# Kernel tuning notes

Hardware: AMD Instinct MI355X
Metric: run time of the kernel (lower is better)

## Reference

```python
import jax, jax.numpy as jnp
import numpy as np

N_HEADS = 4


def setup_inputs() -> dict:
    key = jax.random.key(0)
    ks = jax.random.split(key, 8)
    T, B, V, F = 30, 64, 32, 128   # len_pred, batch, n_vehicles, feature_size
    L, LF, TH = 64, 64, 20         # n_lanes, lane_feature_size, len_hist
    vehicles = jax.random.normal(ks[0], (T, B, V, F), dtype=jnp.float32)
    lanes = jax.random.normal(ks[1], (B, V, L, LF), dtype=jnp.float32)
    mask_lanes = jax.random.randint(ks[2], (TH, B, V, L), 0, 2).astype(bool)
    # torch Linear weight layout [out, in]; conv 1x1 weights squeezed to [out, in]
    Wk = jax.random.normal(ks[3], (F, LF), dtype=jnp.float32) / np.sqrt(LF)
    Wv = jax.random.normal(ks[4], (F, LF), dtype=jnp.float32) / np.sqrt(LF)
    Wq = jax.random.normal(ks[5], (F, F), dtype=jnp.float32) / np.sqrt(F)
    Wc = jax.random.normal(ks[6], (F, F), dtype=jnp.float32) / np.sqrt(F)
    return {"vehicles": vehicles, "lanes": lanes, "mask_lanes": mask_lanes,
            "Wk": Wk, "Wv": Wv, "Wq": Wq, "Wc": Wc}


def reference(vehicles, lanes, mask_lanes, Wk, Wv, Wq, Wc):
    # vehicles: [T,B,V,F], lanes: [B,V,L,LF], mask_lanes: [TH,B,V,L] bool
    T, B, V, F = vehicles.shape
    L = lanes.shape[2]
    H = N_HEADS
    hd = F // H
    # Linear projections of lanes (torch Linear: y = x @ W.T)
    k = jnp.einsum('bvlf,gf->bvlg', lanes, Wk).reshape(B, V, L, H, hd)
    v = jnp.einsum('bvlf,gf->bvlg', lanes, Wv).reshape(B, V, L, H, hd)
    # 1x1 Conv2d on feature channels == per-position linear
    q = jnp.einsum('tbvf,gf->tbvg', vehicles, Wq).reshape(T, B, V, H, hd)
    # mask: any over history dim -> [B,V,L] (the second any in attention is a no-op
    # since the mask is repeated identically over T and heads)
    mask = jnp.any(mask_lanes, axis=0)  # [B,V,L]
    scores = jnp.einsum('tbvhd,bvlhd->tbvhl', q, k) / jnp.sqrt(jnp.float32(hd))
    scores = jnp.where(mask[None, :, :, None, :], scores, jnp.float32(-1e9))
    p = jax.nn.softmax(scores, axis=-1)  # [T,B,V,H,L]
    out = jnp.einsum('tbvhl,bvlhd->tbvhd', p, v).reshape(T, B, V, F)
    out = jnp.einsum('tbvf,gf->tbvg', out, Wc) + vehicles
    return out
```

## Files before the change

kernel.cpp:

```cpp
#include <hip/hip_runtime.h>

#define T_  30
#define B_  64
#define V_  32
#define F_  128
#define L_  64
#define LF_ 64
#define TH_ 20
#define H_  4
#define HD_ 32

typedef __attribute__((ext_vector_type(8))) short bf16x8;
typedef __attribute__((ext_vector_type(4))) float f32x4;
#define MFMA(a,b,c) __builtin_amdgcn_mfma_f32_16x16x32_bf16(a, b, c, 0, 0, 0)

__device__ __forceinline__ float bf1(unsigned short u) {
    unsigned int x = ((unsigned int)u) << 16; float f; __builtin_memcpy(&f, &x, 4); return f;
}
__device__ __forceinline__ unsigned short f2bf(float f) {
    unsigned int x; __builtin_memcpy(&x, &f, 4);
    x += 0x7fffu + ((x >> 16) & 1u);
    return (unsigned short)(x >> 16);
}
__device__ __forceinline__ float4 ld4(const void* p, int idx4, bool isBf16) {
    if (isBf16) {
        ushort4 u = ((const ushort4*)p)[idx4];
        return make_float4(bf1(u.x), bf1(u.y), bf1(u.z), bf1(u.w));
    }
    return ((const float4*)p)[idx4];
}
__device__ __forceinline__ void st4bf(unsigned short* p, f32x4 v) {
    ushort4 u = { f2bf(v[0]), f2bf(v[1]), f2bf(v[2]), f2bf(v[3]) };
    *(ushort4*)p = u;
}
__device__ __forceinline__ bf16x8 ldWfrag(const void* W, int off, bool isBf16) {
    if (isBf16) return *(const bf16x8*)((const unsigned short*)W + off);
    const float* p = (const float*)W + off;
    float4 a = *(const float4*)p;
    float4 b = *(const float4*)(p + 4);
    bf16x8 r;
    r[0] = (short)f2bf(a.x); r[1] = (short)f2bf(a.y);
    r[2] = (short)f2bf(a.z); r[3] = (short)f2bf(a.w);
    r[4] = (short)f2bf(b.x); r[5] = (short)f2bf(b.y);
    r[6] = (short)f2bf(b.z); r[7] = (short)f2bf(b.w);
    return r;
}

__global__ __launch_bounds__(256, 2)
void lane_attn_kernel(const void* __restrict__ veh,
                      const void* __restrict__ lanes,
                      const void* __restrict__ maskp,
                      const void* __restrict__ Wk, const void* __restrict__ Wv,
                      const void* __restrict__ Wq, const void* __restrict__ Wc,
                      float* __restrict__ outp)
{
    const int bv   = blockIdx.x;
    const int tid  = threadIdx.x;
    const int w    = tid >> 6;
    const int lane = tid & 63;
    const int quad = lane >> 4;
    const int lm   = lane & 15;
    const int fbase = w * 32;

    __shared__ __align__(16) unsigned short sRegion[13824];
    __shared__ __align__(16) unsigned short sK [64 * 136];
    __shared__ __align__(16) unsigned short sVt[128 * 72];
    unsigned short* sQ     = sRegion;
    unsigned short* sO     = sRegion;
    unsigned short* sLanes = sRegion + 4352;
    unsigned short* sVehB  = sRegion + 9472;
    unsigned short* sS     = sRegion + 4352;

    const unsigned short* vh16 = (const unsigned short*)veh;
    const int field = (vh16[2 * lane] >> 7) & 0xFF;
    const bool isBf16 = __popcll(__ballot(field >= 100 && field <= 130)) >= 32;
    const unsigned char* mbp = (const unsigned char*)maskp;
    const bool maskByte = (__ballot(mbp[4 * lane + 1] != 0) != 0ULL);

    bool ok;
    {
        const int* mi = (const int*)maskp;
        int o = 0;
        #pragma unroll
        for (int th = 0; th < TH_; ++th) {
            const size_t e = (size_t)th * (B_ * V_ * L_) + (size_t)bv * L_ + lane;
            o |= maskByte ? (int)mbp[e] : mi[e];
        }
        ok = (o != 0);
    }

    bf16x8 wbK[2][2], wbV[2][2], wq[4][2];
    #pragma unroll
    for (int kt = 0; kt < 2; ++kt)
        #pragma unroll
        for (int nt = 0; nt < 2; ++nt) {
            const int off = (fbase + nt * 16 + lm) * 64 + kt * 32 + quad * 8;
            wbK[kt][nt] = ldWfrag(Wk, off, isBf16);
            wbV[kt][nt] = ldWfrag(Wv, off, isBf16);
        }
    #pragma unroll
    for (int kt = 0; kt < 4; ++kt)
        #pragma unroll
        for (int nt = 0; nt < 2; ++nt)
            wq[kt][nt] = ldWfrag(Wq, (fbase + nt * 16 + lm) * 128 + kt * 32 + quad * 8, isBf16);

    for (int u = tid; u < 64 * 16; u += 256) {
        const int l = u >> 4, c4 = u & 15;
        float4 x = ld4(lanes, bv * (L_ * LF_ / 4) + u, isBf16);
        ushort4 y = { f2bf(x.x), f2bf(x.y), f2bf(x.z), f2bf(x.w) };
        *(ushort4*)&sLanes[l * 80 + c4 * 4] = y;
    }
    for (int u = tid; u < 32 * 32; u += 256) {
        const int t = u >> 5, c4 = u & 31;
        ushort4 y = {0, 0, 0, 0};
        if (t < T_) {
            float4 x = ld4(veh, (t * (B_ * V_) + bv) * (F_ / 4) + c4, isBf16);
            y.x = f2bf(x.x); y.y = f2bf(x.y); y.z = f2bf(x.z); y.w = f2bf(x.w);
        }
        *(ushort4*)&sVehB[t * 136 + c4 * 4] = y;
    }
    __syncthreads();

    {
        f32x4 accK[2][4], accV[2][4];
        #pragma unroll
        for (int nt = 0; nt < 2; ++nt)
            #pragma unroll
            for (int mt = 0; mt < 4; ++mt) { accK[nt][mt] = (f32x4)0.f; accV[nt][mt] = (f32x4)0.f; }
        #pragma unroll
        for (int kt = 0; kt < 2; ++kt) {
            bf16x8 a[4];
            #pragma unroll
            for (int mt = 0; mt < 4; ++mt)
                a[mt] = *(const bf16x8*)&sLanes[(mt * 16 + lm) * 80 + kt * 32 + quad * 8];
            #pragma unroll
            for (int nt = 0; nt < 2; ++nt)
                #pragma unroll
                for (int mt = 0; mt < 4; ++mt) {
                    accK[nt][mt] = MFMA(a[mt], wbK[kt][nt], accK[nt][mt]);
                    accV[nt][mt] = MFMA(a[mt], wbV[kt][nt], accV[nt][mt]);
                }
        }
        #pragma unroll
        for (int nt = 0; nt < 2; ++nt) {
            const int f = fbase + nt * 16 + lm;
            #pragma unroll
            for (int mt = 0; mt < 4; ++mt) {
                const int l0 = mt * 16 + quad * 4;
                #pragma unroll
                for (int r = 0; r < 4; ++r) sK[(l0 + r) * 136 + f] = f2bf(accK[nt][mt][r]);
                st4bf(&sVt[f * 72 + l0], accV[nt][mt]);
            }
        }
    }

    {
        f32x4 acc[2][2];
        #pragma unroll
        for (int nt = 0; nt < 2; ++nt)
            #pragma unroll
            for (int mt = 0; mt < 2; ++mt) acc[nt][mt] = (f32x4)0.f;
        #pragma unroll
        for (int kt = 0; kt < 4; ++kt) {
            bf16x8 a[2];
            #pragma unroll
            for (int mt = 0; mt < 2; ++mt)
                a[mt] = *(const bf16x8*)&sVehB[(mt * 16 + lm) * 136 + kt * 32 + quad * 8];
            #pragma unroll
            for (int nt = 0; nt < 2; ++nt)
                #pragma unroll
                for (int mt = 0; mt < 2; ++mt) acc[nt][mt] = MFMA(a[mt], wq[kt][nt], acc[nt][mt]);
        }
        const float sc = 0.17677669529663687f;
        #pragma unroll
        for (int nt = 0; nt < 2; ++nt) {
            const int g = fbase + nt * 16 + lm;
            #pragma unroll
            for (int mt = 0; mt < 2; ++mt) {
                const int t0 = mt * 16 + quad * 4;
                #pragma unroll
                for (int r = 0; r < 4; ++r) sQ[(t0 + r) * 136 + g] = f2bf(acc[nt][mt][r] * sc);
            }
        }
    }

    bf16x8 wc[4][2];
    #pragma unroll
    for (int kt = 0; kt < 4; ++kt)
        #pragma unroll
        for (int nt = 0; nt < 2; ++nt)
            wc[kt][nt] = ldWfrag(Wc, (fbase + nt * 16 + lm) * 128 + kt * 32 + quad * 8, isBf16);

    __syncthreads();

    {
        bf16x8 a[4], b[2];
        #pragma unroll
        for (int mt = 0; mt < 4; ++mt)
            a[mt] = *(const bf16x8*)&sK[(mt * 16 + lm) * 136 + fbase + quad * 8];
        #pragma unroll
        for (int nt = 0; nt < 2; ++nt)
            b[nt] = *(const bf16x8*)&sQ[(nt * 16 + lm) * 136 + fbase + quad * 8];
        #pragma unroll
        for (int mt = 0; mt < 4; ++mt)
            #pragma unroll
            for (int nt = 0; nt < 2; ++nt) {
                f32x4 acc = MFMA(a[mt], b[nt], (f32x4)0.f);
                const int t = nt * 16 + lm;
                st4bf(&sS[(w * 32 + t) * 72 + mt * 16 + quad * 4], acc);
            }
    }

    {
        #pragma unroll
        for (int t = 0; t < T_; ++t) {
            const int idx = (w * 32 + t) * 72 + lane;
            const float p = ok ? __expf(bf1(sS[idx])) : 0.f;
            sS[idx] = f2bf(p);
        }
        sS[(w * 32 + 30) * 72 + lane] = 0;
        sS[(w * 32 + 31) * 72 + lane] = 0;
    }

    {
        bf16x8 bones;
        #pragma unroll
        for (int j = 0; j < 8; ++j) bones[j] = (short)0x3F80;
        f32x4 acc[2][2], ssum[2];
        #pragma unroll
        for (int mt = 0; mt < 2; ++mt) {
            ssum[mt] = (f32x4)0.f;
            #pragma unroll
            for (int nt = 0; nt < 2; ++nt) acc[mt][nt] = (f32x4)0.f;
        }
        #pragma unroll
        for (int kt = 0; kt < 2; ++kt) {
            bf16x8 a[2], b[2];
            #pragma unroll
            for (int mt = 0; mt < 2; ++mt)
                a[mt] = *(const bf16x8*)&sS[(w * 32 + mt * 16 + lm) * 72 + kt * 32 + quad * 8];
            #pragma unroll
            for (int nt = 0; nt < 2; ++nt)
                b[nt] = *(const bf16x8*)&sVt[(fbase + nt * 16 + lm) * 72 + kt * 32 + quad * 8];
            #pragma unroll
            for (int mt = 0; mt < 2; ++mt) {
                ssum[mt] = MFMA(a[mt], bones, ssum[mt]);
                #pragma unroll
                for (int nt = 0; nt < 2; ++nt) acc[mt][nt] = MFMA(a[mt], b[nt], acc[mt][nt]);
            }
        }
        #pragma unroll
        for (int mt = 0; mt < 2; ++mt)
            #pragma unroll
            for (int r = 0; r < 4; ++r) {
                const float s = ssum[mt][r];
                const float inv = (s > 0.f) ? 1.f / s : 0.f;
                const int t = mt * 16 + quad * 4 + r;
                #pragma unroll
                for (int nt = 0; nt < 2; ++nt)
                    sO[t * 136 + fbase + nt * 16 + lm] = f2bf(acc[mt][nt][r] * inv);
            }
    }

    float res[2][2][4];
    #pragma unroll
    for (int nt = 0; nt < 2; ++nt) {
        const int g = fbase + nt * 16 + lm;
        #pragma unroll
        for (int mt = 0; mt < 2; ++mt)
            #pragma unroll
            for (int r = 0; r < 4; ++r) {
                const int t = mt * 16 + quad * 4 + r;
                float v = 0.f;
                if (t < T_) {
                    const size_t off = ((size_t)t * (B_ * V_) + bv) * F_ + g;
                    v = isBf16 ? bf1(((const unsigned short*)veh)[off])
                               : ((const float*)veh)[off];
                }
                res[nt][mt][r] = v;
            }
    }
    __syncthreads();

    {
        f32x4 acc[2][2];
        #pragma unroll
        for (int nt = 0; nt < 2; ++nt)
            #pragma unroll
            for (int mt = 0; mt < 2; ++mt) acc[nt][mt] = (f32x4)0.f;
        #pragma unroll
        for (int kt = 0; kt < 4; ++kt) {
            bf16x8 a[2];
            #pragma unroll
            for (int mt = 0; mt < 2; ++mt)
                a[mt] = *(const bf16x8*)&sO[(mt * 16 + lm) * 136 + kt * 32 + quad * 8];
            #pragma unroll
            for (int nt = 0; nt < 2; ++nt)
                #pragma unroll
                for (int mt = 0; mt < 2; ++mt) acc[nt][mt] = MFMA(a[mt], wc[kt][nt], acc[nt][mt]);
        }
        #pragma unroll
        for (int nt = 0; nt < 2; ++nt) {
            const int g = fbase + nt * 16 + lm;
            #pragma unroll
            for (int mt = 0; mt < 2; ++mt)
                #pragma unroll
                for (int r = 0; r < 4; ++r) {
                    const int t = mt * 16 + quad * 4 + r;
                    if (t < T_) {
                        const size_t off = ((size_t)t * (B_ * V_) + bv) * F_ + g;
                        outp[off] = acc[nt][mt][r] + res[nt][mt][r];
                    }
                }
        }
    }
}

extern "C" void kernel_launch(void* const* d_in, const int* in_sizes, int n_in,
                              void* d_out, int out_size, void* d_ws, size_t ws_size,
                              hipStream_t stream) {
    (void)in_sizes; (void)n_in; (void)out_size; (void)d_ws; (void)ws_size;
    lane_attn_kernel<<<dim3(B_ * V_), dim3(256), 0, stream>>>(
        d_in[0], d_in[1], d_in[2], d_in[3], d_in[4], d_in[5], d_in[6],
        (float*)d_out);
}
```

Baseline: 186.3 us.

## Restructure lane attention into per-wave private smem with swizzled layouts and fewer barriers

Each wave now loads its MFMA operand fragments for lanes and vehicles straight from global memory instead of staging them through shared memory. K, Q, V and probabilities go into per-wave XOR-swizzled shared buffers, which removes the first barrier and avoids bank conflicts. The softmax exponent is applied directly on the score accumulators using a ballot mask, removing a shared-memory round trip. Shared memory shrinks and launch bounds rise to 4 blocks per CU. The risks are redundant global loads, since each wave reloads the same lanes and vehicles tiles, and register pressure from the higher occupancy target.

```diff
diff --git a/kernel.cpp b/kernel.cpp
--- a/kernel.cpp
+++ b/kernel.cpp
@@ -1,4 +1,5 @@
 #include <hip/hip_runtime.h>
+#include <hip/hip_bf16.h>
 
 #define T_  30
 #define B_  64
@@ -22,31 +23,20 @@
     x += 0x7fffu + ((x >> 16) & 1u);
     return (unsigned short)(x >> 16);
 }
-__device__ __forceinline__ float4 ld4(const void* p, int idx4, bool isBf16) {
-    if (isBf16) {
-        ushort4 u = ((const ushort4*)p)[idx4];
-        return make_float4(bf1(u.x), bf1(u.y), bf1(u.z), bf1(u.w));
-    }
-    return ((const float4*)p)[idx4];
-}
-__device__ __forceinline__ void st4bf(unsigned short* p, f32x4 v) {
-    ushort4 u = { f2bf(v[0]), f2bf(v[1]), f2bf(v[2]), f2bf(v[3]) };
-    *(ushort4*)p = u;
-}
-__device__ __forceinline__ bf16x8 ldWfrag(const void* W, int off, bool isBf16) {
-    if (isBf16) return *(const bf16x8*)((const unsigned short*)W + off);
-    const float* p = (const float*)W + off;
-    float4 a = *(const float4*)p;
-    float4 b = *(const float4*)(p + 4);
-    bf16x8 r;
-    r[0] = (short)f2bf(a.x); r[1] = (short)f2bf(a.y);
-    r[2] = (short)f2bf(a.z); r[3] = (short)f2bf(a.w);
-    r[4] = (short)f2bf(b.x); r[5] = (short)f2bf(b.y);
-    r[6] = (short)f2bf(b.z); r[7] = (short)f2bf(b.w);
-    return r;
-}
-
-__global__ __launch_bounds__(256, 2)
+__device__ __forceinline__ unsigned int pkbf(float a, float b) {
+    __hip_bfloat162 h = __float22bfloat162_rn(make_float2(a, b));
+    unsigned int u; __builtin_memcpy(&u, &h, 4); return u;
+}
+__device__ __forceinline__ bf16x8 ldfrag(const void* p, size_t elem, bool isBf16) {
+    if (isBf16) return *(const bf16x8*)((const unsigned short*)p + elem);
+    const float* f = (const float*)p + elem;
+    float4 a = *(const float4*)f;
+    float4 b = *(const float4*)(f + 4);
+    uint4 u = { pkbf(a.x, a.y), pkbf(a.z, a.w), pkbf(b.x, b.y), pkbf(b.z, b.w) };
+    bf16x8 r; __builtin_memcpy(&r, &u, 16); return r;
+}
+
+__global__ __launch_bounds__(256, 4)
 void lane_attn_kernel(const void* __restrict__ veh,
                       const void* __restrict__ lanes,
                       const void* __restrict__ maskp,
@@ -62,22 +52,17 @@
     const int lm   = lane & 15;
     const int fbase = w * 32;
 
-    __shared__ __align__(16) unsigned short sRegion[13824];
-    __shared__ __align__(16) unsigned short sK [64 * 136];
-    __shared__ __align__(16) unsigned short sVt[128 * 72];
-    unsigned short* sQ     = sRegion;
-    unsigned short* sO     = sRegion;
-    unsigned short* sLanes = sRegion + 4352;
-    unsigned short* sVehB  = sRegion + 9472;
-    unsigned short* sS     = sRegion + 4352;
+    __shared__ __align__(16) unsigned short S[20480];
+    const int kb = w * 3072, qb = kb + 2048, vb = 12288 + w * 2048;
+    const int pb = kb, ob = 12288;
 
     const unsigned short* vh16 = (const unsigned short*)veh;
-    const int field = (vh16[2 * lane] >> 7) & 0xFF;
-    const bool isBf16 = __popcll(__ballot(field >= 100 && field <= 130)) >= 32;
+    const int fld = (vh16[2 * lane] >> 7) & 0xFF;
+    const bool isBf16 = __popcll(__ballot(fld >= 100 && fld <= 130)) >= 32;
     const unsigned char* mbp = (const unsigned char*)maskp;
     const bool maskByte = (__ballot(mbp[4 * lane + 1] != 0) != 0ULL);
 
-    bool ok;
+    unsigned long long okmask;
     {
         const int* mi = (const int*)maskp;
         int o = 0;
@@ -86,75 +71,88 @@
             const size_t e = (size_t)th * (B_ * V_ * L_) + (size_t)bv * L_ + lane;
             o |= maskByte ? (int)mbp[e] : mi[e];
         }
-        ok = (o != 0);
-    }
-
-    bf16x8 wbK[2][2], wbV[2][2], wq[4][2];
-    #pragma unroll
-    for (int kt = 0; kt < 2; ++kt)
-        #pragma unroll
-        for (int nt = 0; nt < 2; ++nt) {
-            const int off = (fbase + nt * 16 + lm) * 64 + kt * 32 + quad * 8;
-            wbK[kt][nt] = ldWfrag(Wk, off, isBf16);
-            wbV[kt][nt] = ldWfrag(Wv, off, isBf16);
-        }
-    #pragma unroll
-    for (int kt = 0; kt < 4; ++kt)
-        #pragma unroll
-        for (int nt = 0; nt < 2; ++nt)
-            wq[kt][nt] = ldWfrag(Wq, (fbase + nt * 16 + lm) * 128 + kt * 32 + quad * 8, isBf16);
-
-    for (int u = tid; u < 64 * 16; u += 256) {
-        const int l = u >> 4, c4 = u & 15;
-        float4 x = ld4(lanes, bv * (L_ * LF_ / 4) + u, isBf16);
-        ushort4 y = { f2bf(x.x), f2bf(x.y), f2bf(x.z), f2bf(x.w) };
-        *(ushort4*)&sLanes[l * 80 + c4 * 4] = y;
-    }
-    for (int u = tid; u < 32 * 32; u += 256) {
-        const int t = u >> 5, c4 = u & 31;
-        ushort4 y = {0, 0, 0, 0};
-        if (t < T_) {
-            float4 x = ld4(veh, (t * (B_ * V_) + bv) * (F_ / 4) + c4, isBf16);
-            y.x = f2bf(x.x); y.y = f2bf(x.y); y.z = f2bf(x.z); y.w = f2bf(x.w);
-        }
-        *(ushort4*)&sVehB[t * 136 + c4 * 4] = y;
-    }
-    __syncthreads();
-
-    {
-        f32x4 accK[2][4], accV[2][4];
-        #pragma unroll
-        for (int nt = 0; nt < 2; ++nt)
-            #pragma unroll
-            for (int mt = 0; mt < 4; ++mt) { accK[nt][mt] = (f32x4)0.f; accV[nt][mt] = (f32x4)0.f; }
+        okmask = __ballot(o != 0);
+    }
+
+    {
+        bf16x8 wb[2][2];
+        #pragma unroll
+        for (int kt = 0; kt < 2; ++kt)
+            #pragma unroll
+            for (int nt = 0; nt < 2; ++nt)
+                wb[kt][nt] = ldfrag(Wk, (size_t)(fbase + nt * 16 + lm) * LF_ + kt * 32 + quad * 8, isBf16);
+        f32x4 acc[2][4];
+        #pragma unroll
+        for (int nt = 0; nt < 2; ++nt)
+            #pragma unroll
+            for (int mt = 0; mt < 4; ++mt) acc[nt][mt] = (f32x4)0.f;
         #pragma unroll
         for (int kt = 0; kt < 2; ++kt) {
             bf16x8 a[4];
             #pragma unroll
             for (int mt = 0; mt < 4; ++mt)
-                a[mt] = *(const bf16x8*)&sLanes[(mt * 16 + lm) * 80 + kt * 32 + quad * 8];
-            #pragma unroll
-            for (int nt = 0; nt < 2; ++nt)
-                #pragma unroll
-                for (int mt = 0; mt < 4; ++mt) {
-                    accK[nt][mt] = MFMA(a[mt], wbK[kt][nt], accK[nt][mt]);
-                    accV[nt][mt] = MFMA(a[mt], wbV[kt][nt], accV[nt][mt]);
-                }
-        }
-        #pragma unroll
-        for (int nt = 0; nt < 2; ++nt) {
-            const int f = fbase + nt * 16 + lm;
-            #pragma unroll
-            for (int mt = 0; mt < 4; ++mt) {
-                const int l0 = mt * 16 + quad * 4;
-                #pragma unroll
-                for (int r = 0; r < 4; ++r) sK[(l0 + r) * 136 + f] = f2bf(accK[nt][mt][r]);
-                st4bf(&sVt[f * 72 + l0], accV[nt][mt]);
-            }
-        }
-    }
-
-    {
+                a[mt] = ldfrag(lanes, (size_t)(bv * L_ + mt * 16 + lm) * LF_ + kt * 32 + quad * 8, isBf16);
+            #pragma unroll
+            for (int nt = 0; nt < 2; ++nt)
+                #pragma unroll
+                for (int mt = 0; mt < 4; ++mt) acc[nt][mt] = MFMA(a[mt], wb[kt][nt], acc[nt][mt]);
+        }
+        #pragma unroll
+        for (int nt = 0; nt < 2; ++nt) {
+            const int chunkc = nt * 2 + (lm >> 3);
+            #pragma unroll
+            for (int mt = 0; mt < 4; ++mt)
+                #pragma unroll
+                for (int r = 0; r < 4; ++r) {
+                    const int l = mt * 16 + quad * 4 + r;
+                    S[kb + l * 32 + ((chunkc ^ (l & 3)) << 3) + (lm & 7)] = f2bf(acc[nt][mt][r]);
+                }
+        }
+    }
+    {
+        bf16x8 wb[2][2];
+        #pragma unroll
+        for (int kt = 0; kt < 2; ++kt)
+            #pragma unroll
+            for (int nt = 0; nt < 2; ++nt)
+                wb[kt][nt] = ldfrag(Wv, (size_t)(fbase + nt * 16 + lm) * LF_ + kt * 32 + quad * 8, isBf16);
+        f32x4 acc[2][4];
+        #pragma unroll
+        for (int nt = 0; nt < 2; ++nt)
+            #pragma unroll
+            for (int mt = 0; mt < 4; ++mt) acc[nt][mt] = (f32x4)0.f;
+        #pragma unroll
+        for (int kt = 0; kt < 2; ++kt) {
+            bf16x8 a[4];
+            #pragma unroll
+            for (int mt = 0; mt < 4; ++mt)
+                a[mt] = ldfrag(lanes, (size_t)(bv * L_ + mt * 16 + lm) * LF_ + kt * 32 + quad * 8, isBf16);
+            #pragma unroll
+            for (int nt = 0; nt < 2; ++nt)
+                #pragma unroll
+                for (int mt = 0; mt < 4; ++mt) acc[nt][mt] = MFMA(a[mt], wb[kt][nt], acc[nt][mt]);
+        }
+        #pragma unroll
+        for (int nt = 0; nt < 2; ++nt) {
+            const int dd = nt * 16 + lm;
+            #pragma unroll
+            for (int mt = 0; mt < 4; ++mt)
+                #pragma unroll
+                for (int jp = 0; jp < 2; ++jp) {
+                    const int l0 = mt * 16 + quad * 4 + jp * 2;
+                    *(unsigned int*)&S[vb + dd * 64 + (((l0 >> 3) ^ (dd & 7)) << 3) + (l0 & 7)]
+                        = pkbf(acc[nt][mt][jp * 2], acc[nt][mt][jp * 2 + 1]);
+                }
+        }
+    }
+
+    {
+        bf16x8 wq[4][2];
+        #pragma unroll
+        for (int kt = 0; kt < 4; ++kt)
+            #pragma unroll
+            for (int nt = 0; nt < 2; ++nt)
+                wq[kt][nt] = ldfrag(Wq, (size_t)(fbase + nt * 16 + lm) * F_ + kt * 32 + quad * 8, isBf16);
         f32x4 acc[2][2];
         #pragma unroll
         for (int nt = 0; nt < 2; ++nt)
@@ -164,91 +162,110 @@
         for (int kt = 0; kt < 4; ++kt) {
             bf16x8 a[2];
             #pragma unroll
+            for (int mt = 0; mt < 2; ++mt) {
+                const int t = mt * 16 + lm;
+                const int tc = (t < T_) ? t : (T_ - 1);
+                a[mt] = ldfrag(veh, (size_t)(tc * (B_ * V_) + bv) * F_ + kt * 32 + quad * 8, isBf16);
+            }
+            #pragma unroll
+            for (int nt = 0; nt < 2; ++nt)
+                #pragma unroll
+                for (int mt = 0; mt < 2; ++mt) acc[nt][mt] = MFMA(a[mt], wq[kt][nt], acc[nt][mt]);
+        }
+        const float scl = 0.17677669529663687f;
+        #pragma unroll
+        for (int nt = 0; nt < 2; ++nt) {
+            const int chunkc = nt * 2 + (lm >> 3);
+            #pragma unroll
             for (int mt = 0; mt < 2; ++mt)
-                a[mt] = *(const bf16x8*)&sVehB[(mt * 16 + lm) * 136 + kt * 32 + quad * 8];
-            #pragma unroll
-            for (int nt = 0; nt < 2; ++nt)
-                #pragma unroll
-                for (int mt = 0; mt < 2; ++mt) acc[nt][mt] = MFMA(a[mt], wq[kt][nt], acc[nt][mt]);
-        }
-        const float sc = 0.17677669529663687f;
-        #pragma unroll
-        for (int nt = 0; nt < 2; ++nt) {
-            const int g = fbase + nt * 16 + lm;
+                #pragma unroll
+                for (int r = 0; r < 4; ++r) {
+                    const int t = mt * 16 + quad * 4 + r;
+                    S[qb + t * 32 + ((chunkc ^ r) << 3) + (lm & 7)] = f2bf(acc[nt][mt][r] * scl);
+                }
+        }
+    }
+
+    f32x4 sacc[4][2];
+    {
+        bf16x8 a[4], b[2];
+        #pragma unroll
+        for (int mt = 0; mt < 4; ++mt) {
+            const int l = mt * 16 + lm;
+            a[mt] = *(const bf16x8*)&S[kb + l * 32 + ((quad ^ (l & 3)) << 3)];
+        }
+        #pragma unroll
+        for (int nt = 0; nt < 2; ++nt) {
+            const int t = nt * 16 + lm;
+            b[nt] = *(const bf16x8*)&S[qb + t * 32 + ((quad ^ (t & 3)) << 3)];
+        }
+        #pragma unroll
+        for (int mt = 0; mt < 4; ++mt)
+            #pragma unroll
+            for (int nt = 0; nt < 2; ++nt) sacc[mt][nt] = MFMA(a[mt], b[nt], (f32x4)0.f);
+    }
+
+    {
+        #pragma unroll
+        for (int nt = 0; nt < 2; ++nt) {
+            const int t = nt * 16 + lm;
+            const bool tok = (t < T_);
+            #pragma unroll
+            for (int mt = 0; mt < 4; ++mt)
+                #pragma unroll
+                for (int jp = 0; jp < 2; ++jp) {
+                    const int l0 = mt * 16 + quad * 4 + jp * 2;
+                    const float p0 = (tok && ((okmask >> l0) & 1))       ? __expf(sacc[mt][nt][jp * 2])     : 0.f;
+                    const float p1 = (tok && ((okmask >> (l0 + 1)) & 1)) ? __expf(sacc[mt][nt][jp * 2 + 1]) : 0.f;
+                    const int chunk = 2 * mt + (quad >> 1);
+                    *(unsigned int*)&S[pb + t * 64 + ((chunk ^ (t & 7)) << 3) + ((quad & 1) * 4 + jp * 2)]
+                        = pkbf(p0, p1);
+                }
+        }
+    }
+
+    f32x4 pacc[2][2], ssum[2];
+    {
+        bf16x8 bones;
+        #pragma unroll
+        for (int j = 0; j < 8; ++j) bones[j] = (short)0x3F80;
+        #pragma unroll
+        for (int mt = 0; mt < 2; ++mt) {
+            ssum[mt] = (f32x4)0.f;
+            #pragma unroll
+            for (int nt = 0; nt < 2; ++nt) pacc[mt][nt] = (f32x4)0.f;
+        }
+        #pragma unroll
+        for (int kt = 0; kt < 2; ++kt) {
+            bf16x8 a[2], b[2];
             #pragma unroll
             for (int mt = 0; mt < 2; ++mt) {
-                const int t0 = mt * 16 + quad * 4;
-                #pragma unroll
-                for (int r = 0; r < 4; ++r) sQ[(t0 + r) * 136 + g] = f2bf(acc[nt][mt][r] * sc);
-            }
-        }
-    }
-
+                const int t = mt * 16 + lm;
+                a[mt] = *(const bf16x8*)&S[pb + t * 64 + (((kt * 4 + quad) ^ (t & 7)) << 3)];
+            }
+            #pragma unroll
+            for (int nt = 0; nt < 2; ++nt) {
+                const int dd = nt * 16 + lm;
+                b[nt] = *(const bf16x8*)&S[vb + dd * 64 + (((kt * 4 + quad) ^ (dd & 7)) << 3)];
+            }
+            #pragma unroll
+            for (int mt = 0; mt < 2; ++mt) {
+                ssum[mt] = MFMA(a[mt], bones, ssum[mt]);
+                #pragma unroll
+                for (int nt = 0; nt < 2; ++nt) pacc[mt][nt] = MFMA(a[mt], b[nt], pacc[mt][nt]);
+            }
+        }
+    }
     bf16x8 wc[4][2];
     #pragma unroll
     for (int kt = 0; kt < 4; ++kt)
         #pragma unroll
         for (int nt = 0; nt < 2; ++nt)
-            wc[kt][nt] = ldWfrag(Wc, (fbase + nt * 16 + lm) * 128 + kt * 32 + quad * 8, isBf16);
+            wc[kt][nt] = ldfrag(Wc, (size_t)(fbase + nt * 16 + lm) * F_ + kt * 32 + quad * 8, isBf16);
 
     __syncthreads();
 
     {
-        bf16x8 a[4], b[2];
-        #pragma unroll
-        for (int mt = 0; mt < 4; ++mt)
-            a[mt] = *(const bf16x8*)&sK[(mt * 16 + lm) * 136 + fbase + quad * 8];
-        #pragma unroll
-        for (int nt = 0; nt < 2; ++nt)
-            b[nt] = *(const bf16x8*)&sQ[(nt * 16 + lm) * 136 + fbase + quad * 8];
-        #pragma unroll
-        for (int mt = 0; mt < 4; ++mt)
-            #pragma unroll
-            for (int nt = 0; nt < 2; ++nt) {
-                f32x4 acc = MFMA(a[mt], b[nt], (f32x4)0.f);
-                const int t = nt * 16 + lm;
-                st4bf(&sS[(w * 32 + t) * 72 + mt * 16 + quad * 4], acc);
-            }
-    }
-
-    {
-        #pragma unroll
-        for (int t = 0; t < T_; ++t) {
-            const int idx = (w * 32 + t) * 72 + lane;
-            const float p = ok ? __expf(bf1(sS[idx])) : 0.f;
-            sS[idx] = f2bf(p);
-        }
-        sS[(w * 32 + 30) * 72 + lane] = 0;
-        sS[(w * 32 + 31) * 72 + lane] = 0;
-    }
-
-    {
-        bf16x8 bones;
-        #pragma unroll
-        for (int j = 0; j < 8; ++j) bones[j] = (short)0x3F80;
-        f32x4 acc[2][2], ssum[2];
-        #pragma unroll
-        for (int mt = 0; mt < 2; ++mt) {
-            ssum[mt] = (f32x4)0.f;
-            #pragma unroll
-            for (int nt = 0; nt < 2; ++nt) acc[mt][nt] = (f32x4)0.f;
-        }
-        #pragma unroll
-        for (int kt = 0; kt < 2; ++kt) {
-            bf16x8 a[2], b[2];
-            #pragma unroll
-            for (int mt = 0; mt < 2; ++mt)
-                a[mt] = *(const bf16x8*)&sS[(w * 32 + mt * 16 + lm) * 72 + kt * 32 + quad * 8];
-            #pragma unroll
-            for (int nt = 0; nt < 2; ++nt)
-                b[nt] = *(const bf16x8*)&sVt[(fbase + nt * 16 + lm) * 72 + kt * 32 + quad * 8];
-            #pragma unroll
-            for (int mt = 0; mt < 2; ++mt) {
-                ssum[mt] = MFMA(a[mt], bones, ssum[mt]);
-                #pragma unroll
-                for (int nt = 0; nt < 2; ++nt) acc[mt][nt] = MFMA(a[mt], b[nt], acc[mt][nt]);
-            }
-        }
         #pragma unroll
         for (int mt = 0; mt < 2; ++mt)
             #pragma unroll
@@ -257,27 +274,10 @@
                 const float inv = (s > 0.f) ? 1.f / s : 0.f;
                 const int t = mt * 16 + quad * 4 + r;
                 #pragma unroll
-                for (int nt = 0; nt < 2; ++nt)
-                    sO[t * 136 + fbase + nt * 16 + lm] = f2bf(acc[mt][nt][r] * inv);
-            }
-    }
-
-    float res[2][2][4];
-    #pragma unroll
-    for (int nt = 0; nt < 2; ++nt) {
-        const int g = fbase + nt * 16 + lm;
-        #pragma unroll
-        for (int mt = 0; mt < 2; ++mt)
-            #pragma unroll
-            for (int r = 0; r < 4; ++r) {
-                const int t = mt * 16 + quad * 4 + r;
-                float v = 0.f;
-                if (t < T_) {
-                    const size_t off = ((size_t)t * (B_ * V_) + bv) * F_ + g;
-                    v = isBf16 ? bf1(((const unsigned short*)veh)[off])
-                               : ((const float*)veh)[off];
-                }
-                res[nt][mt][r] = v;
+                for (int nt = 0; nt < 2; ++nt) {
+                    const int f = fbase + nt * 16 + lm;
+                    S[ob + t * 128 + (((f >> 3) ^ (t & 15)) << 3) + (lm & 7)] = f2bf(pacc[mt][nt][r] * inv);
+                }
             }
     }
     __syncthreads();
@@ -292,8 +292,10 @@
         for (int kt = 0; kt < 4; ++kt) {
             bf16x8 a[2];
             #pragma unroll
-            for (int mt = 0; mt < 2; ++mt)
-                a[mt] = *(const bf16x8*)&sO[(mt * 16 + lm) * 136 + kt * 32 + quad * 8];
+            for (int mt = 0; mt < 2; ++mt) {
+                const int t = mt * 16 + lm;
+                a[mt] = *(const bf16x8*)&S[ob + t * 128 + (((kt * 4 + quad) ^ (t & 15)) << 3)];
+            }
             #pragma unroll
             for (int nt = 0; nt < 2; ++nt)
                 #pragma unroll
@@ -309,7 +311,9 @@
                     const int t = mt * 16 + quad * 4 + r;
                     if (t < T_) {
                         const size_t off = ((size_t)t * (B_ * V_) + bv) * F_ + g;
-                        outp[off] = acc[nt][mt][r] + res[nt][mt][r];
+                        const float res = isBf16 ? bf1(((const unsigned short*)veh)[off])
+                                                 : ((const float*)veh)[off];
+                        outp[off] = acc[nt][mt][r] + res;
                     }
                 }
         }
```

New measurement: 223.6 us. +20.0%, slower.
